# Kernel tuning notes

Measured on AMD Instinct MI355X. Metric: run time of the kernel, lower is better.

Reference implementation:

```python
import jax, jax.numpy as jnp
import numpy as np

G = 8          # groups
PATCH = 4      # encoder patch conv kernel/stride
MD = 4         # correlation max displacement -> (2*MD+1)^2 = 81 neighbours
BNEPS = 1e-5
LNEPS = 1e-5

# finite-difference gradient kernel (assumed: forward differences on a C-grid)
GRAD_K = jnp.array([[[[0., 0., 0.], [0., -1., 1.], [0., 0., 0.]]],
                    [[[0., 0., 0.], [0., -1., 0.], [0., 1., 0.]]]], dtype=jnp.float32)

def _vort_kernel():
    # assumed 6x6 Biot-Savart-like vorticity->velocity kernel (CalculusOperators not in source)
    c = 2.5
    ys, xs = np.mgrid[0:6, 0:6].astype(np.float32)
    r2 = (ys - c) ** 2 + (xs - c) ** 2
    u = -(ys - c) / (2.0 * np.pi * r2)
    v = (xs - c) / (2.0 * np.pi * r2)
    return jnp.asarray(np.stack([u, v])[:, None])  # [2,1,6,6]
VORT_K = _vort_kernel()

def conv2d(x, w, pad, stride=1):
    return jax.lax.conv_general_dilated(x, w, (stride, stride), [(pad, pad), (pad, pad)],
                                        dimension_numbers=('NCHW', 'OIHW', 'NCHW'))

def bn(x, g, b):
    # inference-mode BatchNorm with running_mean=0, running_var=1
    return x * (g / jnp.sqrt(1.0 + BNEPS))[None, :, None, None] + b[None, :, None, None]

def up2x(x):
    def lerp_axis(x, axis):
        n = x.shape[axis]
        c = jnp.arange(2 * n, dtype=x.dtype) * (n - 1) / (2 * n - 1)
        i0 = jnp.floor(c).astype(jnp.int32)
        i1 = jnp.minimum(i0 + 1, n - 1)
        w = c - i0.astype(x.dtype)
        a0 = jnp.take(x, i0, axis=axis)
        a1 = jnp.take(x, i1, axis=axis)
        shp = [1] * x.ndim; shp[axis] = 2 * n
        w = w.reshape(shp)
        return a0 * (1 - w) + a1 * w
    return lerp_axis(lerp_axis(x, 2), 3)

def double_conv_up(x, w1, g1, b1, w2, g2, b2):
    x = jax.nn.relu(bn(conv2d(up2x(x), w1, 1), g1, b1))
    return jax.nn.relu(bn(conv2d(up2x(x), w2, 1), g2, b2))

@jax.checkpoint
def correlation(f1, f2):
    # PWC-Net style FunctionCorrelation: mean over channels of f1 * shifted f2, 81 shifts
    N, C, H, W = f1.shape
    f2p = jnp.pad(f2, ((0, 0), (0, 0), (MD, MD), (MD, MD)))
    outs = [jnp.mean(f1 * f2p[:, :, dy:dy + H, dx:dx + W], axis=1)
            for dy in range(2 * MD + 1) for dx in range(2 * MD + 1)]
    return jnp.stack(outs, axis=1)  # [N, 81, H, W]

def cgrid_to_motion(u, v, shape):
    mu = (u[:, :, 1:-1, 1:] + u[:, :, 1:-1, :-1]) * 0.5
    mv = (v[:, :, 1:, 1:-1] + v[:, :, :-1, 1:-1]) * 0.5
    m = jnp.concatenate([mu, mv], axis=1)
    h, w = shape
    up = (m.shape[2] - h) // 2
    left = (m.shape[3] - w) // 2
    return m[:, :, up:up + h, left:left + w]

def calc_phi_velocity(phi, shape):
    vel = conv2d(phi, GRAD_K, 1)
    return cgrid_to_motion(vel[:, 0:1, :, :-1], vel[:, 1:2, :-1, :], shape)

def calc_vort_velocity(stream, shape):
    s = stream[:, :, :-1, :-1]
    vel = conv2d(s, VORT_K, 5)  # full-padding conv == conv_transpose of flipped kernel
    return cgrid_to_motion(vel[:, 0:1, 2:-2, 2:-3], vel[:, 1:2, 2:-3, 2:-2], shape)

def bilinear_sample(f, px, py):
    # f [N,C,H,W]; px,py [N,H,W] absolute coords, border clamp
    H, W = f.shape[-2], f.shape[-1]
    px = jnp.clip(px, 0.0, W - 1.0)
    py = jnp.clip(py, 0.0, H - 1.0)
    x0 = jnp.floor(px); y0 = jnp.floor(py)
    wx = (px - x0)[:, None]; wy = (py - y0)[:, None]
    x0i = x0.astype(jnp.int32); y0i = y0.astype(jnp.int32)
    x1i = jnp.minimum(x0i + 1, W - 1); y1i = jnp.minimum(y0i + 1, H - 1)
    gat = jax.vmap(lambda fi, yi, xi: fi[:, yi, xi])
    v00 = gat(f, y0i, x0i); v01 = gat(f, y0i, x1i)
    v10 = gat(f, y1i, x0i); v11 = gat(f, y1i, x1i)
    return (v00 * (1 - wx) + v01 * wx) * (1 - wy) + (v10 * (1 - wx) + v11 * wx) * wy

def warp(f, vel, sign):
    N, _, H, W = f.shape
    ys, xs = jnp.meshgrid(jnp.arange(H, dtype=f.dtype), jnp.arange(W, dtype=f.dtype), indexing='ij')
    return bilinear_sample(f, xs[None] - sign * vel[:, 0], ys[None] - sign * vel[:, 1])

def bfecc_warp(f, vel):
    f1 = warp(f, vel, 1.0)
    fb = warp(f1, vel, -1.0)
    return warp(f + 0.5 * (f - fb), vel, 1.0)

def _forward(prev, next, texture, mask, boundary,
             enc_w, enc_b,
             phi_w1, phi_g1, phi_b1, phi_w2, phi_g2, phi_b2, phi_ow, phi_ob,
             vor_w1, vor_g1, vor_b1, vor_w2, vor_g2, vor_b2, vor_ow, vor_ob,
             phi_weight, vorticity_weight,
             ln_g, ln_b, fc1_w, fc1_b, fc2_w, fc2_b):
    B, C, H, W = prev.shape
    shape = texture.shape[-2:]
    pm = (prev * mask[:, None]).reshape(B * G, C // G, H, W)
    pb = (prev * boundary[:, None]).reshape(B * G, C // G, H, W)
    nm = (next * mask[:, None]).reshape(B * G, C // G, H, W)
    enc = lambda x: conv2d(x, enc_w, 0, PATCH) + enc_b[None, :, None, None]
    f_nm = enc(nm)
    corr = jnp.concatenate([correlation(enc(pm), f_nm), correlation(enc(pb), f_nm)], axis=1)
    phi = (conv2d(double_conv_up(corr, phi_w1, phi_g1, phi_b1, phi_w2, phi_g2, phi_b2), phi_ow, 0)
           + phi_ob[None, :, None, None]) * phi_weight
    vort = (conv2d(double_conv_up(corr, vor_w1, vor_g1, vor_b1, vor_w2, vor_g2, vor_b2), vor_ow, 0)
            + vor_ob[None, :, None, None]) * vorticity_weight * H
    helm = jnp.concatenate([phi, vort], axis=1)  # [B*G, 2, H, W]
    vel_phi = calc_phi_velocity(helm[:, 0:1], shape)
    vel_vort = calc_vort_velocity(helm[:, 1:2], shape)
    vel = vel_phi + vel_vort
    Bt, Ct, Ht, Wt = texture.shape
    tex = texture.reshape(B * G, Ct // G, Ht, Wt)
    pred = bfecc_warp(tex, vel).reshape(B, Ct, Ht, Wt)
    xp = jnp.transpose(pred, (0, 2, 3, 1))  # [B,H,W,C]
    mu = jnp.mean(xp, -1, keepdims=True)
    var = jnp.var(xp, -1, keepdims=True)
    y = (xp - mu) / jnp.sqrt(var + LNEPS) * ln_g + ln_b
    y = jax.nn.gelu(y @ fc1_w.T + fc1_b, approximate=False)
    y = y @ fc2_w.T + fc2_b
    return pred + jnp.transpose(y, (0, 3, 1, 2))

def setup_inputs():
    ks = jax.random.split(jax.random.key(0), 20)
    B, C, H, W = 4, 64, 260, 260
    Ht, Wt = 258, 258
    D = 128           # correlation_dim
    cg = C // G       # 8 channels per group
    ed = 8            # encoder_dim // groups = 64 // 8
    n = lambda i, shp, s=1.0: jax.random.normal(ks[i], shp, jnp.float32) * s
    return {
        'prev': n(0, (B, C, H, W)), 'next': n(1, (B, C, H, W)),
        'texture': n(2, (B, C, Ht, Wt)),
        'mask': jax.random.uniform(ks[3], (B, H, W), jnp.float32),
        'boundary': jax.random.uniform(ks[4], (B, H, W), jnp.float32),
        'enc_w': n(5, (D, cg, PATCH, PATCH), 0.05), 'enc_b': n(6, (D,), 0.02),
        'phi_w1': n(7, (ed, 162, 3, 3), 0.05), 'phi_g1': jnp.ones(ed), 'phi_b1': jnp.zeros(ed),
        'phi_w2': n(8, (ed, ed, 3, 3), 0.05), 'phi_g2': jnp.ones(ed), 'phi_b2': jnp.zeros(ed),
        'phi_ow': n(9, (1, ed, 1, 1), 0.05), 'phi_ob': n(10, (1,), 0.02),
        'vor_w1': n(11, (ed, 162, 3, 3), 0.05), 'vor_g1': jnp.ones(ed), 'vor_b1': jnp.zeros(ed),
        'vor_w2': n(12, (ed, ed, 3, 3), 0.05), 'vor_g2': jnp.ones(ed), 'vor_b2': jnp.zeros(ed),
        'vor_ow': n(13, (1, ed, 1, 1), 0.05), 'vor_ob': n(14, (1,), 0.02),
        'phi_weight': jnp.array([0.5], jnp.float32),
        'vorticity_weight': jnp.array([0.005], jnp.float32),
        'ln_g': jnp.ones(C), 'ln_b': jnp.zeros(C),
        'fc1_w': n(15, (C, C), 0.05), 'fc1_b': n(16, (C,), 0.02),
        'fc2_w': n(17, (C, C), 0.05), 'fc2_b': n(18, (C,), 0.02),
    }

def reference(prev, next, texture, mask, boundary,
              enc_w, enc_b,
              phi_w1, phi_g1, phi_b1, phi_w2, phi_g2, phi_b2, phi_ow, phi_ob,
              vor_w1, vor_g1, vor_b1, vor_w2, vor_g2, vor_b2, vor_ow, vor_ob,
              phi_weight, vorticity_weight,
              ln_g, ln_b, fc1_w, fc1_b, fc2_w, fc2_b):
    return _forward(prev, next, texture, mask, boundary,
                    enc_w, enc_b,
                    phi_w1, phi_g1, phi_b1, phi_w2, phi_g2, phi_b2, phi_ow, phi_ob,
                    vor_w1, vor_g1, vor_b1, vor_w2, vor_g2, vor_b2, vor_ow, vor_ob,
                    phi_weight, vorticity_weight,
                    ln_g, ln_b, fc1_w, fc1_b, fc2_w, fc2_b)
```

## Files before the change

### kernel.cpp

```cpp
#include <hip/hip_runtime.h>
#include <math.h>


#define NIMG 32
#define HW 260
#define HWT 258
#define EG 65
#define EGP (EG*EG)
#define DENC 128
#define PIX_T (HWT*HWT)
#define PIX_H (HW*HW)

__global__ void k_wt(const float* __restrict__ w, float* __restrict__ wt) {
    int e = blockIdx.x * 256 + threadIdx.x;
    if (e < 128 * 128) {
        int d = e >> 7, i = e & 127;
        wt[i * 128 + d] = w[e];
    }
}

__global__ __launch_bounds__(128) void k_enc(
    const float* __restrict__ src,
    const float* __restrict__ mul,
    const float* __restrict__ wt,
    const float* __restrict__ bias,
    float* __restrict__ out)
{
    int xt = blockIdx.x;
    int yo = blockIdx.y;
    int n  = blockIdx.z;
    int bi = n >> 3, g = n & 7;
    int xo0 = xt * 16;
    __shared__ __align__(16) float patch[2048];
    int tid = threadIdx.x;
    const float* sbase = src + (size_t)(bi * 64 + g * 8) * PIX_H;
    const float* mbase = mul + (size_t)bi * PIX_H;
    int row0 = yo * 4, col0 = xo0 * 4;
    for (int e = tid; e < 2048; e += 128) {
        int c = e >> 8, r = (e >> 6) & 3, col = e & 63;
        int gc = col0 + col;
        float v = 0.f;
        if (gc < HW) {
            int off = (row0 + r) * HW + gc;
            v = sbase[(size_t)c * PIX_H + off] * mbase[off];
        }
        patch[e] = v;
    }
    __syncthreads();
    int d = tid;
    float acc[16];
    float bv = bias[d];
#pragma unroll
    for (int p = 0; p < 16; ++p) acc[p] = bv;
    const float4* p4 = (const float4*)patch;
    for (int j = 0; j < 32; ++j) {
        float w0 = wt[(j * 4 + 0) * 128 + d];
        float w1 = wt[(j * 4 + 1) * 128 + d];
        float w2 = wt[(j * 4 + 2) * 128 + d];
        float w3 = wt[(j * 4 + 3) * 128 + d];
#pragma unroll
        for (int p = 0; p < 16; ++p) {
            float4 v = p4[j * 16 + p];
            acc[p] += w0 * v.x + w1 * v.y + w2 * v.z + w3 * v.w;
        }
    }
    size_t ob = ((size_t)(n * EG + yo) * EG + xo0) * 128 + d;
#pragma unroll
    for (int p = 0; p < 16; ++p)
        if (xo0 + p < EG) out[ob + (size_t)p * 128] = acc[p];
}

__global__ __launch_bounds__(128) void k_corr(
    const float* __restrict__ f1,
    const float* __restrict__ f2,
    float* __restrict__ corr,
    int obase)
{
    int bx = blockIdx.x;
    int dy = bx >> 1, xt = bx & 1;
    int y  = blockIdx.y;
    int n  = blockIdx.z;
    int xs = xt ? 33 : 0;
    int nx = xt ? 32 : 33;
    __shared__ __align__(16) float s1[33 * 132];
    __shared__ __align__(16) float s2[41 * 132];
    int tid = threadIdx.x;
    const float4* g1 = (const float4*)(f1 + ((size_t)(n * EG + y) * EG + xs) * 128);
    float4* s1v = (float4*)s1;
    for (int e = tid; e < nx * 32; e += 128) {
        int xl = e >> 5, c4 = e & 31;
        s1v[xl * 33 + c4] = g1[xl * 32 + c4];
    }
    int y2 = y + dy - 4;
    bool yok = (y2 >= 0 && y2 < EG);
    const float4* g2 = (const float4*)(f2 + (yok ? ((size_t)(n * EG + y2) * EG) * 128 : 0));
    float4* s2v = (float4*)s2;
    for (int e = tid; e < 41 * 32; e += 128) {
        int xl = e >> 5, c4 = e & 31;
        int xg = xs - 4 + xl;
        float4 v = make_float4(0.f, 0.f, 0.f, 0.f);
        if (yok && xg >= 0 && xg < EG) v = g2[xg * 32 + c4];
        s2v[xl * 33 + c4] = v;
    }
    __syncthreads();
    int nact = nx * 3;
    if (tid < nact) {
        int q, xl;
        if (xt) { q = tid >> 5; xl = tid & 31; }
        else    { q = tid / 33; xl = tid - q * 33; }
        int dx0 = q * 3;
        float4 a0 = make_float4(0,0,0,0), a1 = a0, a2 = a0;
        const float4* r1 = (const float4*)s1 + xl * 33;
        const float4* r2 = (const float4*)s2 + (xl + dx0) * 33;
#pragma unroll 8
        for (int i = 0; i < 32; ++i) {
            float4 a = r1[i];
            float4 b0 = r2[i], b1 = r2[33 + i], b2 = r2[66 + i];
            a0.x += a.x * b0.x; a0.y += a.y * b0.y; a0.z += a.z * b0.z; a0.w += a.w * b0.w;
            a1.x += a.x * b1.x; a1.y += a.y * b1.y; a1.z += a.z * b1.z; a1.w += a.w * b1.w;
            a2.x += a.x * b2.x; a2.y += a.y * b2.y; a2.z += a.z * b2.z; a2.w += a.w * b2.w;
        }
        float s[3];
        s[0] = (a0.x + a0.y + a0.z + a0.w) * (1.0f / 128.0f);
        s[1] = (a1.x + a1.y + a1.z + a1.w) * (1.0f / 128.0f);
        s[2] = (a2.x + a2.y + a2.z + a2.w) * (1.0f / 128.0f);
#pragma unroll
        for (int m = 0; m < 3; ++m) {
            int o = obase + dy * 9 + dx0 + m;
            corr[(size_t)(n * 162 + o) * EGP + y * EG + xs + xl] = s[m];
        }
    }
}

__global__ __launch_bounds__(128) void k_conv1(
    const float* __restrict__ corr,
    const float* __restrict__ w_phi,
    const float* __restrict__ w_vor,
    const float* __restrict__ g_phi, const float* __restrict__ b_phi,
    const float* __restrict__ g_vor, const float* __restrict__ b_vor,
    float* __restrict__ h1)
{
    int yp = blockIdx.x;
    int n  = blockIdx.y;
    int y0 = yp * 2;
    __shared__ float craw[4 * 9 * 65];
    __shared__ float upc [4 * 9 * 132];
    __shared__ float wch [16 * 81];
    __shared__ float s_xw[132];
    __shared__ int   s_xi0[132];
    __shared__ int   s_xi1[132];
    __shared__ float s_yw[4];
    __shared__ int   s_yj0[4];
    __shared__ int   s_yj1[4];
    __shared__ int   s_yv[4];
    int tid = threadIdx.x;
    int ylo = y0 - 1; if (ylo < 0) ylo = 0;
    int R0 = (int)((float)(ylo * 64) / 129.0f);
    if (tid < 132) {
        int xu = tid - 1;
        if (xu >= 0 && xu <= 129) {
            float cx = (float)(xu * 64) / 129.0f;
            int i0 = (int)cx;
            int i1 = i0 + 1; if (i1 > 64) i1 = 64;
            s_xw[tid] = cx - (float)i0;
            s_xi0[tid] = i0;
            s_xi1[tid] = i1;
        } else { s_xi0[tid] = -1; s_xi1[tid] = 0; s_xw[tid] = 0.f; }
    }
    if (tid >= 132 && tid < 136) {
        int r = tid - 132;
        int yy = y0 - 1 + r;
        if (yy >= 0 && yy <= 129) {
            float cy = (float)(yy * 64) / 129.0f;
            int i0 = (int)cy;
            int i1 = i0 + 1; if (i1 > 64) i1 = 64;
            s_yw[r] = cy - (float)i0;
            s_yj0[r] = i0 - R0;
            s_yj1[r] = i1 - R0;
            s_yv[r] = 1;
        } else { s_yw[r] = 0.f; s_yj0[r] = 0; s_yj1[r] = 0; s_yv[r] = 0; }
    }
    int og = tid / 26, xg = tid - og * 26;
    int x0 = xg * 5;
    float acc[4][2][5] = {};
    for (int cc = 0; cc < 18; ++cc) {
        int cb = cc * 9;
        __syncthreads();
        for (int e = tid; e < 2340; e += 128) {
            int r = e / 585, rem = e - r * 585, ci = rem / 65, xx = rem - ci * 65;
            int R = R0 + r; if (R > 64) R = 64;
            craw[e] = corr[(size_t)(n * 162 + cb + ci) * EGP + R * EG + xx];
        }
        for (int e = tid; e < 1296; e += 128) {
            int t2o = e / 81, rem = e - t2o * 81, ci = rem / 9, k = rem - ci * 9;
            int t2 = t2o >> 3, o = t2o & 7;
            const float* wsrc = t2 ? w_vor : w_phi;
            wch[e] = wsrc[(o * 162 + cb + ci) * 9 + k];
        }
        __syncthreads();
        for (int e = tid; e < 4752; e += 128) {
            int r = e / 1188, rem = e - r * 1188, ci = rem / 132, xx = rem - ci * 132;
            float val = 0.f;
            int xi0 = s_xi0[xx];
            if (s_yv[r] && xi0 >= 0) {
                int xi1 = s_xi1[xx];
                float wx = s_xw[xx];
                const float* c0 = &craw[(s_yj0[r] * 9 + ci) * 65];
                const float* c1 = &craw[(s_yj1[r] * 9 + ci) * 65];
                float a0 = c0[xi0], a1 = c0[xi1];
                float b0 = c1[xi0], b1 = c1[xi1];
                float tp = a0 + wx * (a1 - a0);
                float bt = b0 + wx * (b1 - b0);
                val = tp + s_yw[r] * (bt - tp);
            }
            upc[e] = val;
        }
        __syncthreads();
        if (tid < 104) {
            for (int ci = 0; ci < 9; ++ci) {
                float u[4][7];
#pragma unroll
                for (int r = 0; r < 4; ++r)
#pragma unroll
                    for (int m = 0; m < 7; ++m)
                        u[r][m] = upc[(r * 9 + ci) * 132 + x0 + m];
#pragma unroll
                for (int o4 = 0; o4 < 4; ++o4) {
                    const float* wp = &wch[(og * 4 + o4) * 81 + ci * 9];
#pragma unroll
                    for (int ky = 0; ky < 3; ++ky)
#pragma unroll
                        for (int kx = 0; kx < 3; ++kx) {
                            float w = wp[ky * 3 + kx];
#pragma unroll
                            for (int yi = 0; yi < 2; ++yi)
#pragma unroll
                                for (int xi = 0; xi < 5; ++xi)
                                    acc[o4][yi][xi] += w * u[ky + yi][xi + kx];
                        }
                }
            }
        }
    }
    if (tid < 104) {
        const float bnsc = 1.0f / sqrtf(1.0f + 1e-5f);
#pragma unroll
        for (int o4 = 0; o4 < 4; ++o4) {
            int t2o = og * 4 + o4, t2 = t2o >> 3, o = t2o & 7;
            float gsc = (t2 ? g_vor[o] : g_phi[o]) * bnsc;
            float bia = (t2 ? b_vor[o] : b_phi[o]);
            size_t pb = (size_t)((t2 * 32 + n) * 8 + o) * 16900;
#pragma unroll
            for (int yi = 0; yi < 2; ++yi)
#pragma unroll
                for (int xi = 0; xi < 5; ++xi) {
                    float v = acc[o4][yi][xi] * gsc + bia;
                    h1[pb + (size_t)(y0 + yi) * 130 + (x0 + xi)] = fmaxf(v, 0.f);
                }
        }
    }
}

__global__ __launch_bounds__(256) void k_conv2(
    const float* __restrict__ h1,
    const float* __restrict__ w_phi2, const float* __restrict__ w_vor2,
    const float* __restrict__ g_phi2, const float* __restrict__ b_phi2,
    const float* __restrict__ g_vor2, const float* __restrict__ b_vor2,
    const float* __restrict__ ow_phi, const float* __restrict__ ob_phi,
    const float* __restrict__ ow_vor, const float* __restrict__ ob_vor,
    const float* __restrict__ phi_weight, const float* __restrict__ vort_weight,
    float* __restrict__ helm)
{
    int y = blockIdx.x, n = blockIdx.y;
    __shared__ float hraw[8320];
    __shared__ float wch[1152];
    __shared__ float bns[16], bnb[16], owv[16], obv[2], wm[2];
    int tid = threadIdx.x;
    int ylo = y - 1; if (ylo < 0) ylo = 0;
    int R0 = (int)((float)(ylo * 129) / 259.0f);
    for (int e = tid; e < 8320; e += 256) {
        int t2 = e / 4160, rem = e - t2 * 4160;
        int j = rem / 1040, rem2 = rem - j * 1040;
        int ci = rem2 / 130, xx = rem2 - ci * 130;
        int R = R0 + j; if (R > 129) R = 129;
        hraw[e] = h1[(size_t)((t2 * 32 + n) * 8 + ci) * 16900 + R * 130 + xx];
    }
    for (int e = tid; e < 1152; e += 256) {
        int t2 = e / 576, rem = e - t2 * 576;
        int o = rem / 72, rem2 = rem - o * 72;
        int ci = rem2 / 9, k = rem2 - ci * 9;
        wch[e] = (t2 ? w_vor2 : w_phi2)[(o * 8 + ci) * 9 + k];
    }
    if (tid < 16) {
        int t2 = tid >> 3, o = tid & 7;
        bns[tid] = (t2 ? g_vor2[o] : g_phi2[o]) * (1.0f / sqrtf(1.0f + 1e-5f));
        bnb[tid] = (t2 ? b_vor2[o] : b_phi2[o]);
        owv[tid] = (t2 ? ow_vor[o] : ow_phi[o]);
    }
    if (tid == 0) {
        obv[0] = ob_phi[0]; obv[1] = ob_vor[0];
        wm[0] = phi_weight[0]; wm[1] = vort_weight[0] * 260.0f;
    }
    __syncthreads();
    for (int x = tid; x < HW; x += 256) {
        float wy[3]; int rj0[3], rj1[3]; bool vy[3];
#pragma unroll
        for (int ky = 0; ky < 3; ++ky) {
            int yy = y - 1 + ky;
            vy[ky] = (yy >= 0 && yy < HW);
            if (vy[ky]) {
                float cy = (float)(yy * 129) / 259.0f;
                int i0 = (int)cy; wy[ky] = cy - (float)i0;
                int i1 = i0 + 1; if (i1 > 129) i1 = 129;
                rj0[ky] = i0 - R0; rj1[ky] = i1 - R0;
            } else { wy[ky] = 0; rj0[ky] = 0; rj1[ky] = 0; }
        }
        float wxv[3]; int c0[3], c1[3]; bool vx[3];
#pragma unroll
        for (int kx = 0; kx < 3; ++kx) {
            int xxp = x - 1 + kx;
            vx[kx] = (xxp >= 0 && xxp < HW);
            if (vx[kx]) {
                float cx = (float)(xxp * 129) / 259.0f;
                int i0 = (int)cx; wxv[kx] = cx - (float)i0;
                int i1 = i0 + 1; if (i1 > 129) i1 = 129;
                c0[kx] = i0; c1[kx] = i1;
            } else { wxv[kx] = 0; c0[kx] = 0; c1[kx] = 0; }
        }
        float res[2];
#pragma unroll
        for (int t2 = 0; t2 < 2; ++t2) {
            float acc[8] = {0,0,0,0,0,0,0,0};
            for (int ci = 0; ci < 8; ++ci) {
#pragma unroll
                for (int ky = 0; ky < 3; ++ky) {
                    if (!vy[ky]) continue;
                    const float* r0p = &hraw[((t2 * 4 + rj0[ky]) * 8 + ci) * 130];
                    const float* r1p = &hraw[((t2 * 4 + rj1[ky]) * 8 + ci) * 130];
                    float u3[3];
#pragma unroll
                    for (int kx = 0; kx < 3; ++kx) {
                        if (vx[kx]) {
                            float tp = r0p[c0[kx]] + wxv[kx] * (r0p[c1[kx]] - r0p[c0[kx]]);
                            float bt = r1p[c0[kx]] + wxv[kx] * (r1p[c1[kx]] - r1p[c0[kx]]);
                            u3[kx] = tp + wy[ky] * (bt - tp);
                        } else u3[kx] = 0.f;
                    }
#pragma unroll
                    for (int o = 0; o < 8; ++o) {
                        const float* wp = &wch[((t2 * 8 + o) * 8 + ci) * 9 + ky * 3];
                        acc[o] += wp[0] * u3[0] + wp[1] * u3[1] + wp[2] * u3[2];
                    }
                }
            }
            float dot = 0.f;
#pragma unroll
            for (int o = 0; o < 8; ++o) {
                float hv = fmaxf(acc[o] * bns[t2 * 8 + o] + bnb[t2 * 8 + o], 0.f);
                dot += owv[t2 * 8 + o] * hv;
            }
            res[t2] = (dot + obv[t2]) * wm[t2];
        }
        helm[(size_t)(n * 2 + 0) * PIX_H + y * HW + x] = res[0];
        helm[(size_t)(n * 2 + 1) * PIX_H + y * HW + x] = res[1];
    }
}

__device__ __forceinline__ float K0f(int a, int b) {
    if (a < 0 || a > 5 || b < 0 || b > 5) return 0.f;
    float fa = (float)a - 2.5f, fb = (float)b - 2.5f;
    float r2 = fa * fa + fb * fb;
    return -fa / (6.28318530717958647692f * r2);
}
__device__ __forceinline__ float K1f(int a, int b) {
    if (a < 0 || a > 5 || b < 0 || b > 5) return 0.f;
    float fa = (float)a - 2.5f, fb = (float)b - 2.5f;
    float r2 = fa * fa + fb * fb;
    return fb / (6.28318530717958647692f * r2);
}

__global__ __launch_bounds__(256) void k_vel(
    const float* __restrict__ helm, float* __restrict__ vel)
{
    int idx = blockIdx.x * 256 + threadIdx.x;
    if (idx >= NIMG * PIX_T) return;
    int n = idx / PIX_T, pix = idx - n * PIX_T;
    int yy = pix / HWT, xx = pix - yy * HWT;
    const float* phi = helm + (size_t)(n * 2) * PIX_H;
    const float* s   = helm + (size_t)(n * 2 + 1) * PIX_H;
    float sv[7][7];
#pragma unroll
    for (int di = 0; di < 7; ++di) {
        int i = yy + di - 3;
#pragma unroll
        for (int dj = 0; dj < 7; ++dj) {
            int j = xx + dj - 3;
            sv[di][dj] = (i >= 0 && i < 259 && j >= 0 && j < 259) ? s[i * HW + j] : 0.f;
        }
    }
    float ax = 0.5f * (phi[(yy + 1) * HW + xx + 2] - phi[(yy + 1) * HW + xx]);
#pragma unroll
    for (int a = 0; a < 6; ++a)
#pragma unroll
        for (int d = 0; d < 7; ++d) {
            float coef = K0f(a, d) + K0f(a, d - 1);
            ax += 0.5f * coef * sv[a + 1][d];
        }
    float ay = 0.5f * (phi[(yy + 2) * HW + xx + 1] - phi[yy * HW + xx + 1]);
#pragma unroll
    for (int d = 0; d < 7; ++d)
#pragma unroll
        for (int b = 0; b < 6; ++b) {
            float coef = K1f(d, b) + K1f(d - 1, b);
            ay += 0.5f * coef * sv[d][b + 1];
        }
    vel[(size_t)(n * 2) * PIX_T + pix]     = ax;
    vel[(size_t)(n * 2 + 1) * PIX_T + pix] = ay;
}

__device__ __forceinline__ float bsample(const float* __restrict__ plane,
                                         float px, float py) {
    px = fminf(fmaxf(px, 0.f), 257.f);
    py = fminf(fmaxf(py, 0.f), 257.f);
    float fx = floorf(px), fy = floorf(py);
    int x0 = (int)fx, y0 = (int)fy;
    float wx = px - fx, wy = py - fy;
    int x1 = x0 + 1; if (x1 > 257) x1 = 257;
    int y1 = y0 + 1; if (y1 > 257) y1 = 257;
    const float* r0 = plane + y0 * HWT;
    const float* r1 = plane + y1 * HWT;
    float v00 = r0[x0], v01 = r0[x1], v10 = r1[x0], v11 = r1[x1];
    float tp = v00 + wx * (v01 - v00);
    float bt = v10 + wx * (v11 - v10);
    return tp + wy * (bt - tp);
}

__global__ __launch_bounds__(256) void k_warp(
    const float* __restrict__ src,
    const float* __restrict__ vel,
    float sign,
    const float* __restrict__ tex,
    int mode,
    float* __restrict__ out)
{
    int idx = blockIdx.x * 256 + threadIdx.x;
    if (idx >= NIMG * 8 * PIX_T) return;
    int plane_i = idx / PIX_T;
    int pix = idx - plane_i * PIX_T;
    int n = plane_i >> 3;
    int y = pix / HWT, x = pix - y * HWT;
    float vx = vel[(size_t)(n * 2) * PIX_T + pix];
    float vy = vel[(size_t)(n * 2 + 1) * PIX_T + pix];
    const float* plane = src + (size_t)plane_i * PIX_T;
    float v = bsample(plane, (float)x - sign * vx, (float)y - sign * vy);
    if (mode) v = 1.5f * tex[idx] - 0.5f * v;
    out[idx] = v;
}

__global__ __launch_bounds__(256, 2) void k_lnmlp(
    float* __restrict__ out,
    const float* __restrict__ lng, const float* __restrict__ lnb,
    const float* __restrict__ w1, const float* __restrict__ b1,
    const float* __restrict__ w2, const float* __restrict__ b2)
{
    int yy = blockIdx.x, b = blockIdx.y;
    __shared__ __align__(16) float sw1[4096];
    __shared__ __align__(16) float sw2t[4096];
    __shared__ float sb1[64], sb2[64], sg[64], sbt[64];
    int tid = threadIdx.x;
    for (int e = tid; e < 4096; e += 256) {
        sw1[e] = w1[e];
        sw2t[(e & 63) * 64 + (e >> 6)] = w2[e];
    }
    if (tid < 64) { sb1[tid] = b1[tid]; sb2[tid] = b2[tid]; sg[tid] = lng[tid]; sbt[tid] = lnb[tid]; }
    __syncthreads();
    float* base = out + (size_t)b * 64 * PIX_T + (size_t)yy * HWT;
    for (int x = tid; x < HWT; x += 256) {
        float sum = 0.f, sumsq = 0.f;
        for (int k = 0; k < 64; ++k) {
            float v = base[(size_t)k * PIX_T + x];
            sum += v; sumsq += v * v;
        }
        float mu = sum * (1.0f / 64.0f);
        float var = sumsq * (1.0f / 64.0f) - mu * mu;
        float inv = 1.0f / sqrtf(var + 1e-5f);
        float xn[64];
#pragma unroll
        for (int k = 0; k < 64; ++k) {
            float v = base[(size_t)k * PIX_T + x];
            xn[k] = (v - mu) * inv * sg[k] + sbt[k];
        }
        float acc2[64];
#pragma unroll
        for (int j2 = 0; j2 < 64; ++j2) acc2[j2] = 0.f;
        for (int j = 0; j < 64; ++j) {
            float t = sb1[j];
            const float4* wrow = (const float4*)&sw1[j * 64];
#pragma unroll
            for (int k4 = 0; k4 < 16; ++k4) {
                float4 w = wrow[k4];
                t += xn[4 * k4] * w.x + xn[4 * k4 + 1] * w.y
                   + xn[4 * k4 + 2] * w.z + xn[4 * k4 + 3] * w.w;
            }
            float hj = 0.5f * t * (1.0f + erff(t * 0.70710678118654752f));
            const float4* w2row = (const float4*)&sw2t[j * 64];
#pragma unroll
            for (int q = 0; q < 16; ++q) {
                float4 w = w2row[q];
                acc2[4 * q]     += hj * w.x;
                acc2[4 * q + 1] += hj * w.y;
                acc2[4 * q + 2] += hj * w.z;
                acc2[4 * q + 3] += hj * w.w;
            }
        }
#pragma unroll
        for (int j2 = 0; j2 < 64; ++j2)
            base[(size_t)j2 * PIX_T + x] += sb2[j2] + acc2[j2];
    }
}

extern "C" void kernel_launch(void* const* d_in, const int* in_sizes, int n_in,
                              void* d_out, int out_size, void* d_ws, size_t ws_size,
                              hipStream_t stream) {
    const float* prev       = (const float*)d_in[0];
    const float* next       = (const float*)d_in[1];
    const float* texture    = (const float*)d_in[2];
    const float* mask       = (const float*)d_in[3];
    const float* boundary   = (const float*)d_in[4];
    const float* enc_w      = (const float*)d_in[5];
    const float* enc_b      = (const float*)d_in[6];
    const float* phi_w1     = (const float*)d_in[7];
    const float* phi_g1     = (const float*)d_in[8];
    const float* phi_b1     = (const float*)d_in[9];
    const float* phi_w2     = (const float*)d_in[10];
    const float* phi_g2     = (const float*)d_in[11];
    const float* phi_b2     = (const float*)d_in[12];
    const float* phi_ow     = (const float*)d_in[13];
    const float* phi_ob     = (const float*)d_in[14];
    const float* vor_w1     = (const float*)d_in[15];
    const float* vor_g1     = (const float*)d_in[16];
    const float* vor_b1     = (const float*)d_in[17];
    const float* vor_w2     = (const float*)d_in[18];
    const float* vor_g2     = (const float*)d_in[19];
    const float* vor_b2     = (const float*)d_in[20];
    const float* vor_ow     = (const float*)d_in[21];
    const float* vor_ob     = (const float*)d_in[22];
    const float* phi_weight = (const float*)d_in[23];
    const float* vor_weight = (const float*)d_in[24];
    const float* ln_g       = (const float*)d_in[25];
    const float* ln_b       = (const float*)d_in[26];
    const float* fc1_w      = (const float*)d_in[27];
    const float* fc1_b      = (const float*)d_in[28];
    const float* fc2_w      = (const float*)d_in[29];
    const float* fc2_b      = (const float*)d_in[30];

    float* ws = (float*)d_ws;
    float* F_NM = ws + 0;
    float* F_A  = ws + 17305600;
    float* CORR = ws + 34611200;
    float* WT   = ws + 56513600;
    float* H1   = ws + 0;
    float* HELM = ws + 17305600;
    float* VEL  = ws + 21632000;
    float* F1B  = ws + 34611200;
    float* F2B  = ws + 0;
    float* OUT  = (float*)d_out;

    k_wt<<<dim3(64), dim3(256), 0, stream>>>(enc_w, WT);

    dim3 encg(5, 65, 32);
    k_enc<<<encg, dim3(128), 0, stream>>>(next, mask, WT, enc_b, F_NM);
    k_enc<<<encg, dim3(128), 0, stream>>>(prev, mask, WT, enc_b, F_A);

    dim3 corrg(18, 65, 32);
    k_corr<<<corrg, dim3(128), 0, stream>>>(F_A, F_NM, CORR, 0);
    k_enc<<<encg, dim3(128), 0, stream>>>(prev, boundary, WT, enc_b, F_A);
    k_corr<<<corrg, dim3(128), 0, stream>>>(F_A, F_NM, CORR, 81);

    k_conv1<<<dim3(65, 32), dim3(128), 0, stream>>>(
        CORR, phi_w1, vor_w1, phi_g1, phi_b1, vor_g1, vor_b1, H1);

    k_conv2<<<dim3(260, 32), dim3(256), 0, stream>>>(
        H1, phi_w2, vor_w2, phi_g2, phi_b2, vor_g2, vor_b2,
        phi_ow, phi_ob, vor_ow, vor_ob, phi_weight, vor_weight, HELM);

    int nv = NIMG * PIX_T;
    k_vel<<<dim3((nv + 255) / 256), dim3(256), 0, stream>>>(HELM, VEL);

    int nw = NIMG * 8 * PIX_T;
    int wb = (nw + 255) / 256;
    k_warp<<<dim3(wb), dim3(256), 0, stream>>>(texture, VEL,  1.0f, texture, 0, F1B);
    k_warp<<<dim3(wb), dim3(256), 0, stream>>>(F1B,     VEL, -1.0f, texture, 1, F2B);
    k_warp<<<dim3(wb), dim3(256), 0, stream>>>(F2B,     VEL,  1.0f, texture, 0, OUT);

    k_lnmlp<<<dim3(258, 4), dim3(256), 0, stream>>>(
        OUT, ln_g, ln_b, fc1_w, fc1_b, fc2_w, fc2_b);
}
```

Baseline: 3.460 ms.

## Retile conv1 to four output rows per block with 256 threads

The first decoder conv kernel now computes four output rows per block with 256 threads, where 208 threads each handle one phi and one vorticity output channel. Input channels are processed in chunks of 6 instead of 9. The shared-memory staging of raw correlation rows is removed, and the bilinear upsample now reads the correlation directly from global memory through the read-only cache. The aim is to use more threads per block, reuse each upsampled row across more output rows, and halve the number of blocks, at the cost of more global gathers per upsampled value and 48 idle threads per block.

Measured after the change: 3.075 ms. 1.13x faster.

```diff
diff --git a/kernel.cpp b/kernel.cpp
--- a/kernel.cpp
+++ b/kernel.cpp
@@ -132,7 +132,7 @@
     }
 }
 
-__global__ __launch_bounds__(128) void k_conv1(
+__global__ __launch_bounds__(256) void k_conv1(
     const float* __restrict__ corr,
     const float* __restrict__ w_phi,
     const float* __restrict__ w_vor,
@@ -142,20 +142,17 @@
 {
     int yp = blockIdx.x;
     int n  = blockIdx.y;
-    int y0 = yp * 2;
-    __shared__ float craw[4 * 9 * 65];
-    __shared__ float upc [4 * 9 * 132];
-    __shared__ float wch [16 * 81];
+    int y0 = yp * 4;
+    __shared__ float upc[6 * 6 * 132];
+    __shared__ float wch[16 * 6 * 9];
     __shared__ float s_xw[132];
     __shared__ int   s_xi0[132];
     __shared__ int   s_xi1[132];
-    __shared__ float s_yw[4];
-    __shared__ int   s_yj0[4];
-    __shared__ int   s_yj1[4];
-    __shared__ int   s_yv[4];
+    __shared__ float s_yw[6];
+    __shared__ int   s_yj0[6];
+    __shared__ int   s_yj1[6];
+    __shared__ int   s_yv[6];
     int tid = threadIdx.x;
-    int ylo = y0 - 1; if (ylo < 0) ylo = 0;
-    int R0 = (int)((float)(ylo * 64) / 129.0f);
     if (tid < 132) {
         int xu = tid - 1;
         if (xu >= 0 && xu <= 129) {
@@ -167,7 +164,7 @@
             s_xi1[tid] = i1;
         } else { s_xi0[tid] = -1; s_xi1[tid] = 0; s_xw[tid] = 0.f; }
     }
-    if (tid >= 132 && tid < 136) {
+    if (tid >= 132 && tid < 138) {
         int r = tid - 132;
         int yy = y0 - 1 + r;
         if (yy >= 0 && yy <= 129) {
@@ -175,88 +172,91 @@
             int i0 = (int)cy;
             int i1 = i0 + 1; if (i1 > 64) i1 = 64;
             s_yw[r] = cy - (float)i0;
-            s_yj0[r] = i0 - R0;
-            s_yj1[r] = i1 - R0;
+            s_yj0[r] = i0;
+            s_yj1[r] = i1;
             s_yv[r] = 1;
         } else { s_yw[r] = 0.f; s_yj0[r] = 0; s_yj1[r] = 0; s_yv[r] = 0; }
     }
     int og = tid / 26, xg = tid - og * 26;
     int x0 = xg * 5;
-    float acc[4][2][5] = {};
-    for (int cc = 0; cc < 18; ++cc) {
-        int cb = cc * 9;
+    bool act = (og < 8);
+    float acc[2][4][5] = {};
+    for (int cc = 0; cc < 27; ++cc) {
+        int cb = cc * 6;
         __syncthreads();
-        for (int e = tid; e < 2340; e += 128) {
-            int r = e / 585, rem = e - r * 585, ci = rem / 65, xx = rem - ci * 65;
-            int R = R0 + r; if (R > 64) R = 64;
-            craw[e] = corr[(size_t)(n * 162 + cb + ci) * EGP + R * EG + xx];
-        }
-        for (int e = tid; e < 1296; e += 128) {
-            int t2o = e / 81, rem = e - t2o * 81, ci = rem / 9, k = rem - ci * 9;
-            int t2 = t2o >> 3, o = t2o & 7;
-            const float* wsrc = t2 ? w_vor : w_phi;
-            wch[e] = wsrc[(o * 162 + cb + ci) * 9 + k];
-        }
-        __syncthreads();
-        for (int e = tid; e < 4752; e += 128) {
-            int r = e / 1188, rem = e - r * 1188, ci = rem / 132, xx = rem - ci * 132;
+        for (int e = tid; e < 4752; e += 256) {
+            int r = e / 792, rem = e - r * 792, ci = rem / 132, xx = rem - ci * 132;
             float val = 0.f;
             int xi0 = s_xi0[xx];
             if (s_yv[r] && xi0 >= 0) {
+                const float* cp = corr + (size_t)(n * 162 + cb + ci) * EGP;
+                int J0 = s_yj0[r] * 65, J1 = s_yj1[r] * 65;
                 int xi1 = s_xi1[xx];
-                float wx = s_xw[xx];
-                const float* c0 = &craw[(s_yj0[r] * 9 + ci) * 65];
-                const float* c1 = &craw[(s_yj1[r] * 9 + ci) * 65];
-                float a0 = c0[xi0], a1 = c0[xi1];
-                float b0 = c1[xi0], b1 = c1[xi1];
-                float tp = a0 + wx * (a1 - a0);
-                float bt = b0 + wx * (b1 - b0);
+                float wxv = s_xw[xx];
+                float a0 = __ldg(cp + J0 + xi0), a1 = __ldg(cp + J0 + xi1);
+                float b0 = __ldg(cp + J1 + xi0), b1 = __ldg(cp + J1 + xi1);
+                float tp = a0 + wxv * (a1 - a0);
+                float bt = b0 + wxv * (b1 - b0);
                 val = tp + s_yw[r] * (bt - tp);
             }
             upc[e] = val;
         }
+        for (int e = tid; e < 864; e += 256) {
+            int oc = e / 54, rem = e - oc * 54, ci = rem / 9, k = rem - ci * 9;
+            int t2 = oc >> 3, o = oc & 7;
+            wch[e] = (t2 ? w_vor : w_phi)[(o * 162 + cb + ci) * 9 + k];
+        }
         __syncthreads();
-        if (tid < 104) {
-            for (int ci = 0; ci < 9; ++ci) {
-                float u[4][7];
-#pragma unroll
-                for (int r = 0; r < 4; ++r)
-#pragma unroll
-                    for (int m = 0; m < 7; ++m)
-                        u[r][m] = upc[(r * 9 + ci) * 132 + x0 + m];
-#pragma unroll
-                for (int o4 = 0; o4 < 4; ++o4) {
-                    const float* wp = &wch[(og * 4 + o4) * 81 + ci * 9];
-#pragma unroll
-                    for (int ky = 0; ky < 3; ++ky)
-#pragma unroll
-                        for (int kx = 0; kx < 3; ++kx) {
-                            float w = wp[ky * 3 + kx];
-#pragma unroll
-                            for (int yi = 0; yi < 2; ++yi)
+        if (act) {
+            for (int ci = 0; ci < 6; ++ci) {
+                float wr[2][9];
+#pragma unroll
+                for (int p = 0; p < 2; ++p)
+#pragma unroll
+                    for (int k = 0; k < 9; ++k)
+                        wr[p][k] = wch[((og + 8 * p) * 6 + ci) * 9 + k];
+#pragma unroll
+                for (int r = 0; r < 6; ++r) {
+                    float u7[7];
+                    const float* up = &upc[(r * 6 + ci) * 132 + x0];
+#pragma unroll
+                    for (int m = 0; m < 7; ++m) u7[m] = up[m];
+#pragma unroll
+                    for (int ky = 0; ky < 3; ++ky) {
+                        int yi = r - ky;
+                        if (yi < 0 || yi > 3) continue;
+#pragma unroll
+                        for (int p = 0; p < 2; ++p)
+#pragma unroll
+                            for (int kx = 0; kx < 3; ++kx) {
+                                float w = wr[p][ky * 3 + kx];
 #pragma unroll
                                 for (int xi = 0; xi < 5; ++xi)
-                                    acc[o4][yi][xi] += w * u[ky + yi][xi + kx];
-                        }
+                                    acc[p][yi][xi] += w * u7[xi + kx];
+                            }
+                    }
                 }
             }
         }
     }
-    if (tid < 104) {
+    if (act) {
         const float bnsc = 1.0f / sqrtf(1.0f + 1e-5f);
 #pragma unroll
-        for (int o4 = 0; o4 < 4; ++o4) {
-            int t2o = og * 4 + o4, t2 = t2o >> 3, o = t2o & 7;
-            float gsc = (t2 ? g_vor[o] : g_phi[o]) * bnsc;
-            float bia = (t2 ? b_vor[o] : b_phi[o]);
-            size_t pb = (size_t)((t2 * 32 + n) * 8 + o) * 16900;
-#pragma unroll
-            for (int yi = 0; yi < 2; ++yi)
-#pragma unroll
-                for (int xi = 0; xi < 5; ++xi) {
-                    float v = acc[o4][yi][xi] * gsc + bia;
-                    h1[pb + (size_t)(y0 + yi) * 130 + (x0 + xi)] = fmaxf(v, 0.f);
+        for (int p = 0; p < 2; ++p) {
+            float gsc = (p ? g_vor[og] : g_phi[og]) * bnsc;
+            float bia = (p ? b_vor[og] : b_phi[og]);
+            size_t pb = (size_t)((p * 32 + n) * 8 + og) * 16900;
+#pragma unroll
+            for (int yi = 0; yi < 4; ++yi) {
+                int row = y0 + yi;
+                if (row < 130) {
+#pragma unroll
+                    for (int xi = 0; xi < 5; ++xi) {
+                        float v = acc[p][yi][xi] * gsc + bia;
+                        h1[pb + (size_t)row * 130 + (x0 + xi)] = fmaxf(v, 0.f);
+                    }
                 }
+            }
         }
     }
 }
@@ -577,7 +577,7 @@
     k_enc<<<encg, dim3(128), 0, stream>>>(prev, boundary, WT, enc_b, F_A);
     k_corr<<<corrg, dim3(128), 0, stream>>>(F_A, F_NM, CORR, 81);
 
-    k_conv1<<<dim3(65, 32), dim3(128), 0, stream>>>(
+    k_conv1<<<dim3(33, 32), dim3(256), 0, stream>>>(
         CORR, phi_w1, vor_w1, phi_g1, phi_b1, vor_g1, vor_b1, H1);
 
     k_conv2<<<dim3(260, 32), dim3(256), 0, stream>>>(
```
